# Kernel tuning notes

Measured on AMD Instinct MI355X. Metric: run time of the kernel, lower is better.

Reference implementation:

```python
import jax, jax.numpy as jnp
import numpy as np

POS_SIZE = 63
LATENT_SIZE = 256
NUM_CLUSTERS = 64
N = 524288


def setup_inputs() -> dict:
    key = jax.random.key(0)
    k1, k2, k3, k4 = jax.random.split(key, 4)
    X = jax.random.normal(k1, (N, POS_SIZE + LATENT_SIZE), dtype=jnp.float32)
    cluster_ids = jax.random.randint(k2, (N,), 0, NUM_CLUSTERS, dtype=jnp.int32)
    # nn.Linear weights have shape [out_features, in_features]
    W_pos = jax.random.normal(k3, (3 * NUM_CLUSTERS, POS_SIZE), dtype=jnp.float32) * 0.1
    W_feat = jax.random.normal(k4, (3 * NUM_CLUSTERS, LATENT_SIZE), dtype=jnp.float32) * 0.1
    return {"X": X, "cluster_ids": cluster_ids, "W_pos": W_pos, "W_feat": W_feat}


def reference(X, cluster_ids, W_pos, W_feat):
    # Dense projections: [N, 3*num_clusters]
    rgb_clusters = (
        jnp.einsum("np,cp->nc", X[:, :POS_SIZE], W_pos)
        + jnp.einsum("nl,cl->nc", X[:, POS_SIZE:], W_feat)
    )
    # Per-row gather of the 3 columns belonging to this row's cluster.
    cols = 3 * cluster_ids[:, None] + jnp.arange(3, dtype=cluster_ids.dtype)[None, :]  # [N, 3]
    rgb = jnp.take_along_axis(rgb_clusters, cols, axis=1)  # [N, 3]
    return rgb
```

## Files before the change

### kernel.cpp

```cpp
#include <hip/hip_runtime.h>


constexpr int POS = 63, LAT = 256, DIM = 319, NCH = 192;
constexpr int ROWS = 16;
constexpr int PW_DW = NCH * 160;
constexpr size_t PW_BYTES = (size_t)PW_DW * 4;
constexpr int TILE_DW = ROWS * DIM;
constexpr int TILE_F4 = TILE_DW / 4;
constexpr int GRID = 768;

typedef __attribute__((ext_vector_type(8))) short short8;
typedef __attribute__((ext_vector_type(4))) float f32x4;

__device__ __forceinline__ unsigned f2bf(float f) {
    unsigned u = __float_as_uint(f);
    return (u + 0x7fffu + ((u >> 16) & 1u)) >> 16;
}

__global__ __launch_bounds__(256) void pack_weights(
    const float* __restrict__ Wp, const float* __restrict__ Wf,
    unsigned* __restrict__ pw)
{
    const int idx = blockIdx.x * 256 + threadIdx.x;
    if (idx >= PW_DW) return;
    const int ch = idx / 160, d = idx - ch * 160;
    auto wat = [&](int k) -> float {
        if (k < POS) return Wp[ch * POS + k];
        if (k < DIM) return Wf[ch * LAT + (k - POS)];
        return 0.f;
    };
    pw[idx] = f2bf(wat(2 * d)) | (f2bf(wat(2 * d + 1)) << 16);
}

__global__ __launch_bounds__(256, 3) void lad_mfma3(
    const float4* __restrict__ X4, const int* __restrict__ cid,
    const unsigned* __restrict__ pw, float* __restrict__ out,
    int ntiles, int tpb)
{
    __shared__ float xb[2][TILE_DW];

    const int thr = threadIdx.x;
    const int l   = thr & 63;
    const int wid = thr >> 6;
    const int n0  = wid * 48;
    const int cl  = l & 15;
    const int q   = l >> 4;

    short8 Bf[3][10];
#pragma unroll
    for (int nt = 0; nt < 3; ++nt)
#pragma unroll
        for (int kk = 0; kk < 10; ++kk)
            Bf[nt][kk] = *reinterpret_cast<const short8*>(
                pw + (size_t)(n0 + nt * 16 + cl) * 160 + kk * 16 + q * 4);

    const int t0 = blockIdx.x * tpb;
    const int tend = min(t0 + tpb, ntiles);
    if (t0 >= tend) return;

    auto stage = [&](int tile, int p) {
        const float4* src = X4 + (size_t)tile * TILE_F4;
#pragma unroll
        for (int j = 0; j < 5; ++j) {
            const int slot = j * 256 + thr;
            if (slot < TILE_F4)
                __builtin_amdgcn_global_load_lds(
                    (const __attribute__((address_space(1))) unsigned int*)(src + slot),
                    (__attribute__((address_space(3))) unsigned int*)&xb[p][slot * 4],
                    16, 0, 0);
        }
    };

    stage(t0, 0);
    __syncthreads();

    int p = 0;
    for (int t = t0; t < tend; ++t) {
        if (t + 1 < tend) stage(t + 1, p ^ 1);

        int c3v[4];
#pragma unroll
        for (int j = 0; j < 4; ++j)
            c3v[j] = 3 * cid[(size_t)t * ROWS + q * 4 + j];

        f32x4 acc[3];
#pragma unroll
        for (int nt = 0; nt < 3; ++nt)
            acc[nt] = (f32x4)0.0f;

#pragma unroll
        for (int kk = 0; kk < 10; ++kk) {
            const float* fp = &xb[p][cl * DIM + kk * 32 + q * 8];
            union { unsigned u[4]; short8 s; } cv;
#pragma unroll
            for (int h = 0; h < 4; ++h) {
                asm("v_cvt_pk_bf16_f32 %0, %1, %2"
                    : "=v"(cv.u[h]) : "v"(fp[2 * h]), "v"(fp[2 * h + 1]));
            }
#pragma unroll
            for (int nt = 0; nt < 3; ++nt)
                acc[nt] = __builtin_amdgcn_mfma_f32_16x16x32_bf16(
                    cv.s, Bf[nt][kk], acc[nt], 0, 0, 0);
        }

#pragma unroll
        for (int j = 0; j < 4; ++j) {
            const int grow = t * ROWS + q * 4 + j;
            const int c3 = c3v[j];
#pragma unroll
            for (int nt = 0; nt < 3; ++nt) {
                const int col = n0 + nt * 16 + cl;
                const unsigned d = (unsigned)(col - c3);
                if (d < 3u)
                    out[(size_t)grow * 3 + d] = acc[nt][j];
            }
        }

        __syncthreads();
        p ^= 1;
    }
}

template <int CTRL>
__device__ __forceinline__ float dpp_add_step(float x) {
    int s = __builtin_amdgcn_update_dpp(0, __float_as_int(x), CTRL,
                                        0xF, 0xF, true);
    return x + __int_as_float(s);
}
__device__ __forceinline__ float wave_reduce_sum(float x) {
    x = dpp_add_step<0x111>(x);
    x = dpp_add_step<0x112>(x);
    x = dpp_add_step<0x114>(x);
    x = dpp_add_step<0x118>(x);
    x = dpp_add_step<0x142>(x);
    x = dpp_add_step<0x143>(x);
    return x;
}

__global__ __launch_bounds__(256) void lad_fallback(
    const float* __restrict__ X, const int* __restrict__ cid,
    const float* __restrict__ Wp, const float* __restrict__ Wf,
    float* __restrict__ out, int n)
{
    const int lane = threadIdx.x & 63;
    const int wave = (int)((blockIdx.x * blockDim.x + threadIdx.x) >> 6);
    if (wave >= n) return;
    const size_t row = (size_t)wave;
    const float* xrow = X + row * (size_t)DIM;
    const float* xf   = xrow + POS;
    const int c3 = cid[row] * 3;
    const float* wp0 = Wp + (size_t)c3 * POS;
    const float* wf0 = Wf + (size_t)c3 * LAT;
    float a0 = 0.f, a1 = 0.f, a2 = 0.f;
#pragma unroll
    for (int i = 0; i < 4; ++i) {
        const int k = lane + 64 * i;
        const float x = xf[k];
        a0 = fmaf(x, wf0[k], a0);
        a1 = fmaf(x, wf0[k + LAT], a1);
        a2 = fmaf(x, wf0[k + 2 * LAT], a2);
    }
    if (lane < POS) {
        const float x = xrow[lane];
        a0 = fmaf(x, wp0[lane], a0);
        a1 = fmaf(x, wp0[lane + POS], a1);
        a2 = fmaf(x, wp0[lane + 2 * POS], a2);
    }
    a0 = wave_reduce_sum(a0);
    a1 = wave_reduce_sum(a1);
    a2 = wave_reduce_sum(a2);
    if (lane == 63) {
        float* o = out + row * 3;
        o[0] = a0; o[1] = a1; o[2] = a2;
    }
}

extern "C" void kernel_launch(void* const* d_in, const int* in_sizes, int n_in,
                              void* d_out, int out_size, void* d_ws, size_t ws_size,
                              hipStream_t stream) {
    const float* X   = (const float*)d_in[0];
    const int*   cid = (const int*)d_in[1];
    const float* Wp  = (const float*)d_in[2];
    const float* Wf  = (const float*)d_in[3];
    float* out = (float*)d_out;
    const int n = in_sizes[1];

    if (ws_size >= PW_BYTES && n > 0 && (n % ROWS) == 0) {
        unsigned* pw = (unsigned*)d_ws;
        pack_weights<<<(PW_DW + 255) / 256, 256, 0, stream>>>(Wp, Wf, pw);
        const int ntiles = n / ROWS;
        const int tpb = (ntiles + GRID - 1) / GRID;
        lad_mfma3<<<GRID, 256, 0, stream>>>((const float4*)X, cid, pw, out,
                                            ntiles, tpb);
    } else {
        const int blocks = (n + 3) / 4;
        lad_fallback<<<blocks, 256, 0, stream>>>(X, cid, Wp, Wf, out, n);
    }
}
```

Baseline: 146.8 us.

## Triple-buffer LDS staging with explicit vmcnt waits and fewer blocks

Replaces the double-buffered X tile staging with a three-deep ring of LDS buffers. Each thread now always issues five loads, clamped to a valid address, so that a fixed s_waitcnt vmcnt count can tell when the current tile has landed, and refills run two tiles ahead. Grid drops from 768 to 512 blocks with two blocks per CU to fit the larger LDS footprint. The aim is to hide HBM latency better in this memory-bound projection, at the cost of lower occupancy and some redundant prefetches near the end of each block's range.

Measured after the change: 177.3 us. +20.7%, slower.

```diff
diff --git a/kernel.cpp b/kernel.cpp
--- a/kernel.cpp
+++ b/kernel.cpp
@@ -7,7 +7,8 @@
 constexpr size_t PW_BYTES = (size_t)PW_DW * 4;
 constexpr int TILE_DW = ROWS * DIM;
 constexpr int TILE_F4 = TILE_DW / 4;
-constexpr int GRID = 768;
+constexpr int BUF_DW = 5120;
+constexpr int GRID = 512;
 
 typedef __attribute__((ext_vector_type(8))) short short8;
 typedef __attribute__((ext_vector_type(4))) float f32x4;
@@ -32,12 +33,12 @@
     pw[idx] = f2bf(wat(2 * d)) | (f2bf(wat(2 * d + 1)) << 16);
 }
 
-__global__ __launch_bounds__(256, 3) void lad_mfma3(
+__global__ __launch_bounds__(256, 2) void lad_mfma4(
     const float4* __restrict__ X4, const int* __restrict__ cid,
     const unsigned* __restrict__ pw, float* __restrict__ out,
     int ntiles, int tpb)
 {
-    __shared__ float xb[2][TILE_DW];
+    __shared__ float xb[3][BUF_DW];
 
     const int thr = threadIdx.x;
     const int l   = thr & 63;
@@ -63,20 +64,26 @@
 #pragma unroll
         for (int j = 0; j < 5; ++j) {
             const int slot = j * 256 + thr;
-            if (slot < TILE_F4)
-                __builtin_amdgcn_global_load_lds(
-                    (const __attribute__((address_space(1))) unsigned int*)(src + slot),
-                    (__attribute__((address_space(3))) unsigned int*)&xb[p][slot * 4],
-                    16, 0, 0);
+            const int gs   = slot < TILE_F4 ? slot : TILE_F4 - 1;
+            __builtin_amdgcn_global_load_lds(
+                (const __attribute__((address_space(1))) unsigned int*)(src + gs),
+                (__attribute__((address_space(3))) unsigned int*)&xb[p][slot * 4],
+                16, 0, 0);
         }
     };
 
-    stage(t0, 0);
-    __syncthreads();
-
-    int p = 0;
+    stage(t0,     0);
+    stage(min(t0 + 1, ntiles - 1), 1);
+    stage(min(t0 + 2, ntiles - 1), 2);
+
+    int pi = 0;
     for (int t = t0; t < tend; ++t) {
-        if (t + 1 < tend) stage(t + 1, p ^ 1);
+        asm volatile("s_waitcnt vmcnt(10)" ::: "memory");
+        __builtin_amdgcn_sched_barrier(0);
+        __builtin_amdgcn_s_barrier();
+        __builtin_amdgcn_sched_barrier(0);
+
+        const float* cur = xb[pi];
 
         int c3v[4];
 #pragma unroll
@@ -90,7 +97,7 @@
 
 #pragma unroll
         for (int kk = 0; kk < 10; ++kk) {
-            const float* fp = &xb[p][cl * DIM + kk * 32 + q * 8];
+            const float* fp = &cur[cl * DIM + kk * 32 + q * 8];
             union { unsigned u[4]; short8 s; } cv;
 #pragma unroll
             for (int h = 0; h < 4; ++h) {
@@ -116,9 +123,15 @@
             }
         }
 
-        __syncthreads();
-        p ^= 1;
-    }
+        __builtin_amdgcn_s_barrier();
+        __builtin_amdgcn_sched_barrier(0);
+
+        stage(min(t + 3, ntiles - 1), pi);
+
+        pi = (pi == 2) ? 0 : pi + 1;
+    }
+
+    asm volatile("s_waitcnt vmcnt(0)" ::: "memory");
 }
 
 template <int CTRL>
@@ -185,12 +198,12 @@
     float* out = (float*)d_out;
     const int n = in_sizes[1];
 
-    if (ws_size >= PW_BYTES && n > 0 && (n % ROWS) == 0) {
+    if (ws_size >= PW_BYTES && n > 0 && (n % ROWS) == 0 && n / ROWS >= 4) {
         unsigned* pw = (unsigned*)d_ws;
         pack_weights<<<(PW_DW + 255) / 256, 256, 0, stream>>>(Wp, Wf, pw);
         const int ntiles = n / ROWS;
         const int tpb = (ntiles + GRID - 1) / GRID;
-        lad_mfma3<<<GRID, 256, 0, stream>>>((const float4*)X, cid, pw, out,
+        lad_mfma4<<<GRID, 256, 0, stream>>>((const float4*)X, cid, pw, out,
                                             ntiles, tpb);
     } else {
         const int blocks = (n + 3) / 4;
```
